# Performance work log

Measured on AMD Instinct MI355X. Metric: run time of the kernel, lower is better.

## Reference

```python
import jax, jax.numpy as jnp
import numpy as np

IN_FEATURES = 8192
OUT_FEATURES = 8192
MAX_STATES = 100
THRESHOLD = float(MAX_STATES // 2)  # 50.0


def setup_inputs() -> dict:
    key = jax.random.key(0)
    k1, k2, k3, k4 = jax.random.split(key, 4)
    spike_input = (jax.random.uniform(k1, (1, IN_FEATURES)) < 0.2).astype(jnp.float32)  # sparse binary spikes
    synapse_states = jax.random.uniform(k2, (OUT_FEATURES, IN_FEATURES)) * MAX_STATES  # straddles THRESHOLD
    membrane_potential = jax.random.uniform(k3, (OUT_FEATURES,)) * 3.0
    adaptive_threshold = jnp.full((OUT_FEATURES,), 3.0, dtype=jnp.float32)
    eligibility_trace = jax.random.uniform(k4, (OUT_FEATURES, IN_FEATURES)) * 3.0
    return {
        "spike_input": spike_input,
        "synapse_states": synapse_states,
        "membrane_potential": membrane_potential,
        "adaptive_threshold": adaptive_threshold,
        "eligibility_trace": eligibility_trace,
    }


def reference(spike_input, synapse_states, membrane_potential, adaptive_threshold, eligibility_trace):
    # Ternary (here effectively binary 0/1) weight generation from synapse states
    w = (synapse_states > THRESHOLD).astype(jnp.float32)  # [O, I]
    x = spike_input.reshape(1, -1)                        # [1, I]
    current = (x @ w.T).reshape(-1)                       # [O]

    # LIF membrane update: v <- 0.6*v + I
    v = membrane_potential * 0.6 + current                # [O]
    spikes = (v >= adaptive_threshold).astype(jnp.float32)  # [O]

    # Hebbian eligibility trace: decay, add outer-product, clamp
    trace_new = jnp.clip(
        eligibility_trace * 0.7 + jnp.outer(spikes, x.reshape(-1)),
        0.0, 3.0,
    )  # [O, I]

    # Soft reset of membrane potential where a spike occurred
    v_new = v * (1.0 - spikes) * 0.3                      # [O]

    return spikes, v_new, trace_new
```

## Files before the change

### kernel.cpp

```cpp
#include <hip/hip_runtime.h>


#define IN_F 8192
#define OUT_F 8192
#define SYN_THRESH 50.0f

typedef float vfloat4 __attribute__((ext_vector_type(4)));

__global__ __launch_bounds__(256, 8) void snn_matvec(
    const float* __restrict__ x,
    const float* __restrict__ syn,
    const float* __restrict__ mp,
    const float* __restrict__ thr,
    float* __restrict__ out_spikes,
    float* __restrict__ out_vnew)
{
    const int wave = threadIdx.x >> 6;
    const int lane = threadIdx.x & 63;
    const int row  = (blockIdx.x << 2) | wave;
    const long long base = (long long)row * IN_F;

    const vfloat4* __restrict__ syn4 = (const vfloat4*)(syn + base);
    const vfloat4* __restrict__ x4   = (const vfloat4*)x;

    float sum = 0.0f;
#pragma unroll 1
    for (int c = 0; c < 8; ++c) {
        vfloat4 s[4], xx[4];
#pragma unroll
        for (int u = 0; u < 4; ++u) {
            const int idx = (((c << 2) + u) << 6) | lane;
            s[u]  = __builtin_nontemporal_load(&syn4[idx]);
            xx[u] = x4[idx];
        }
#pragma unroll
        for (int u = 0; u < 4; ++u) {
            sum += ((s[u].x > SYN_THRESH) ? xx[u].x : 0.0f)
                 + ((s[u].y > SYN_THRESH) ? xx[u].y : 0.0f)
                 + ((s[u].z > SYN_THRESH) ? xx[u].z : 0.0f)
                 + ((s[u].w > SYN_THRESH) ? xx[u].w : 0.0f);
        }
    }

#pragma unroll
    for (int off = 32; off > 0; off >>= 1)
        sum += __shfl_xor(sum, off, 64);

    if (lane == 0) {
        const float v     = mp[row] * 0.6f + sum;
        const float spike = (v >= thr[row]) ? 1.0f : 0.0f;
        out_spikes[row] = spike;
        out_vnew[row]   = v * (1.0f - spike) * 0.3f;
    }
}

__global__ __launch_bounds__(256, 8) void snn_trace(
    const float* __restrict__ x,
    const float* __restrict__ trace,
    const float* __restrict__ spikes,
    float* __restrict__ out_trace)
{
    const long long blk4 = (long long)blockIdx.x * 8192;
    const vfloat4* __restrict__ tr4 = (const vfloat4*)trace + blk4;
    vfloat4* __restrict__ ot4       = (vfloat4*)out_trace + blk4;
    const vfloat4* __restrict__ x4  = (const vfloat4*)x;
    const int row0 = blockIdx.x << 2;
    const int tid  = threadIdx.x;

#pragma unroll 1
    for (int c = 0; c < 8; ++c) {
        vfloat4 t[4], xx[4];
        float sp[4];
#pragma unroll
        for (int u = 0; u < 4; ++u) {
            const int idx = (c << 10) | (u << 8) | tid;
            t[u]  = tr4[idx];
            xx[u] = x4[idx & 2047];
            sp[u] = spikes[row0 + (idx >> 11)];
        }
#pragma unroll
        for (int u = 0; u < 4; ++u) {
            const int idx = (c << 10) | (u << 8) | tid;
            vfloat4 o;
            o.x = fminf(fmaxf(fmaf(t[u].x, 0.7f, sp[u] * xx[u].x), 0.0f), 3.0f);
            o.y = fminf(fmaxf(fmaf(t[u].y, 0.7f, sp[u] * xx[u].y), 0.0f), 3.0f);
            o.z = fminf(fmaxf(fmaf(t[u].z, 0.7f, sp[u] * xx[u].z), 0.0f), 3.0f);
            o.w = fminf(fmaxf(fmaf(t[u].w, 0.7f, sp[u] * xx[u].w), 0.0f), 3.0f);
            ot4[idx] = o;
        }
    }
}

extern "C" void kernel_launch(void* const* d_in, const int* in_sizes, int n_in,
                              void* d_out, int out_size, void* d_ws, size_t ws_size,
                              hipStream_t stream) {
    const float* x     = (const float*)d_in[0];
    const float* syn   = (const float*)d_in[1];
    const float* mp    = (const float*)d_in[2];
    const float* thr   = (const float*)d_in[3];
    const float* trace = (const float*)d_in[4];

    float* out = (float*)d_out;
    float* out_spikes = out;
    float* out_vnew   = out + OUT_F;
    float* out_trace  = out + 2 * OUT_F;

    snn_matvec<<<OUT_F / 4, 256, 0, stream>>>(
        x, syn, mp, thr, out_spikes, out_vnew);
    snn_trace<<<OUT_F / 4, 256, 0, stream>>>(
        x, trace, out_spikes, out_trace);
}
```

Before: 585.3 us.

## Replace row-per-wave matvec with grid-strided sweep and atomic row accumulation

The matvec is restructured so every thread strides across the whole synapse matrix with a global stride. Each wave reduces its 256-float chunk and one lane atomically adds the result into a workspace current vector. A small LIF kernel then computes spikes from that vector, and the trace kernel is also converted to the same global grid-stride pattern. The goal is to spread memory streaming more evenly across the grid. In exchange it adds a memset, an extra launch, many atomics (32 per row), and a floating-point summation order that is no longer deterministic.

```diff
diff --git a/kernel.cpp b/kernel.cpp
--- a/kernel.cpp
+++ b/kernel.cpp
@@ -7,86 +7,90 @@
 
 typedef float vfloat4 __attribute__((ext_vector_type(4)));
 
-__global__ __launch_bounds__(256, 8) void snn_matvec(
+#define NF4_TOTAL (1 << 24)
+#define NTHREADS  (1 << 19)
+#define NITER     (NF4_TOTAL / NTHREADS)
+
+__global__ __launch_bounds__(256, 8) void snn_gate_sweep(
     const float* __restrict__ x,
     const float* __restrict__ syn,
+    float* __restrict__ current)
+{
+    const int gtid = blockIdx.x * 256 + threadIdx.x;
+    const int lane = threadIdx.x & 63;
+    const vfloat4* __restrict__ syn4 = (const vfloat4*)syn;
+    const vfloat4* __restrict__ x4   = (const vfloat4*)x;
+
+#pragma unroll 1
+    for (int it = 0; it < NITER; it += 4) {
+        vfloat4 s[4], xx[4];
+        int g[4];
+#pragma unroll
+        for (int u = 0; u < 4; ++u) {
+            g[u]  = gtid + (it + u) * NTHREADS;
+            s[u]  = __builtin_nontemporal_load(&syn4[g[u]]);
+            xx[u] = x4[g[u] & 2047];
+        }
+#pragma unroll
+        for (int u = 0; u < 4; ++u) {
+            float p = ((s[u].x > SYN_THRESH) ? xx[u].x : 0.0f)
+                    + ((s[u].y > SYN_THRESH) ? xx[u].y : 0.0f)
+                    + ((s[u].z > SYN_THRESH) ? xx[u].z : 0.0f)
+                    + ((s[u].w > SYN_THRESH) ? xx[u].w : 0.0f);
+#pragma unroll
+            for (int off = 32; off > 0; off >>= 1)
+                p += __shfl_xor(p, off, 64);
+            if (lane == 0)
+                atomicAdd(&current[g[u] >> 11], p);
+        }
+    }
+}
+
+__global__ __launch_bounds__(256) void snn_lif(
+    const float* __restrict__ current,
     const float* __restrict__ mp,
     const float* __restrict__ thr,
     float* __restrict__ out_spikes,
     float* __restrict__ out_vnew)
 {
-    const int wave = threadIdx.x >> 6;
-    const int lane = threadIdx.x & 63;
-    const int row  = (blockIdx.x << 2) | wave;
-    const long long base = (long long)row * IN_F;
-
-    const vfloat4* __restrict__ syn4 = (const vfloat4*)(syn + base);
-    const vfloat4* __restrict__ x4   = (const vfloat4*)x;
-
-    float sum = 0.0f;
-#pragma unroll 1
-    for (int c = 0; c < 8; ++c) {
-        vfloat4 s[4], xx[4];
-#pragma unroll
-        for (int u = 0; u < 4; ++u) {
-            const int idx = (((c << 2) + u) << 6) | lane;
-            s[u]  = __builtin_nontemporal_load(&syn4[idx]);
-            xx[u] = x4[idx];
-        }
-#pragma unroll
-        for (int u = 0; u < 4; ++u) {
-            sum += ((s[u].x > SYN_THRESH) ? xx[u].x : 0.0f)
-                 + ((s[u].y > SYN_THRESH) ? xx[u].y : 0.0f)
-                 + ((s[u].z > SYN_THRESH) ? xx[u].z : 0.0f)
-                 + ((s[u].w > SYN_THRESH) ? xx[u].w : 0.0f);
-        }
-    }
-
-#pragma unroll
-    for (int off = 32; off > 0; off >>= 1)
-        sum += __shfl_xor(sum, off, 64);
-
-    if (lane == 0) {
-        const float v     = mp[row] * 0.6f + sum;
-        const float spike = (v >= thr[row]) ? 1.0f : 0.0f;
-        out_spikes[row] = spike;
-        out_vnew[row]   = v * (1.0f - spike) * 0.3f;
-    }
+    const int i = blockIdx.x * 256 + threadIdx.x;
+    const float v     = mp[i] * 0.6f + current[i];
+    const float spike = (v >= thr[i]) ? 1.0f : 0.0f;
+    out_spikes[i] = spike;
+    out_vnew[i]   = v * (1.0f - spike) * 0.3f;
 }
 
-__global__ __launch_bounds__(256, 8) void snn_trace(
+__global__ __launch_bounds__(256, 8) void snn_trace_sweep(
     const float* __restrict__ x,
     const float* __restrict__ trace,
     const float* __restrict__ spikes,
     float* __restrict__ out_trace)
 {
-    const long long blk4 = (long long)blockIdx.x * 8192;
-    const vfloat4* __restrict__ tr4 = (const vfloat4*)trace + blk4;
-    vfloat4* __restrict__ ot4       = (vfloat4*)out_trace + blk4;
+    const int gtid = blockIdx.x * 256 + threadIdx.x;
+    const vfloat4* __restrict__ tr4 = (const vfloat4*)trace;
     const vfloat4* __restrict__ x4  = (const vfloat4*)x;
-    const int row0 = blockIdx.x << 2;
-    const int tid  = threadIdx.x;
+    vfloat4* __restrict__ ot4       = (vfloat4*)out_trace;
 
 #pragma unroll 1
-    for (int c = 0; c < 8; ++c) {
+    for (int it = 0; it < NITER; it += 4) {
         vfloat4 t[4], xx[4];
         float sp[4];
+        int g[4];
 #pragma unroll
         for (int u = 0; u < 4; ++u) {
-            const int idx = (c << 10) | (u << 8) | tid;
-            t[u]  = tr4[idx];
-            xx[u] = x4[idx & 2047];
-            sp[u] = spikes[row0 + (idx >> 11)];
+            g[u]  = gtid + (it + u) * NTHREADS;
+            t[u]  = tr4[g[u]];
+            xx[u] = x4[g[u] & 2047];
+            sp[u] = spikes[g[u] >> 11];
         }
 #pragma unroll
         for (int u = 0; u < 4; ++u) {
-            const int idx = (c << 10) | (u << 8) | tid;
             vfloat4 o;
             o.x = fminf(fmaxf(fmaf(t[u].x, 0.7f, sp[u] * xx[u].x), 0.0f), 3.0f);
             o.y = fminf(fmaxf(fmaf(t[u].y, 0.7f, sp[u] * xx[u].y), 0.0f), 3.0f);
             o.z = fminf(fmaxf(fmaf(t[u].z, 0.7f, sp[u] * xx[u].z), 0.0f), 3.0f);
             o.w = fminf(fmaxf(fmaf(t[u].w, 0.7f, sp[u] * xx[u].w), 0.0f), 3.0f);
-            ot4[idx] = o;
+            ot4[g[u]] = o;
         }
     }
 }
@@ -105,8 +109,10 @@
     float* out_vnew   = out + OUT_F;
     float* out_trace  = out + 2 * OUT_F;
 
-    snn_matvec<<<OUT_F / 4, 256, 0, stream>>>(
-        x, syn, mp, thr, out_spikes, out_vnew);
-    snn_trace<<<OUT_F / 4, 256, 0, stream>>>(
-        x, trace, out_spikes, out_trace);
+    float* current = (float*)d_ws;
+
+    hipMemsetAsync(current, 0, OUT_F * sizeof(float), stream);
+    snn_gate_sweep<<<NTHREADS / 256, 256, 0, stream>>>(x, syn, current);
+    snn_lif<<<OUT_F / 256, 256, 0, stream>>>(current, mp, thr, out_spikes, out_vnew);
+    snn_trace_sweep<<<NTHREADS / 256, 256, 0, stream>>>(x, trace, out_spikes, out_trace);
 }
```

Result: slower. 624.7 us (+6.7%).
